# Kernel optimization log

Measured on AMD Instinct MI355X. Metric: run time of the kernel, lower is better.

The kernel has to match this reference:

```python
import jax, jax.numpy as jnp
import numpy as np
import math

S, B, D = 2048, 8, 256
HEADS = 8
DPROJ = 128
DFF = 1024
DH = DPROJ // HEADS  # 16


def _layernorm(x, g, b, eps=1e-5):
    mu = jnp.mean(x, axis=-1, keepdims=True)
    var = jnp.mean((x - mu) ** 2, axis=-1, keepdims=True)
    return (x - mu) * jax.lax.rsqrt(var + eps) * g + b


def setup_inputs() -> dict:
    key = jax.random.key(0)
    ks = jax.random.split(key, 16)
    s = 0.02
    return {
        "src": jax.random.normal(ks[0], (S, B, D), dtype=jnp.float32),
        "Wq": jax.random.normal(ks[1], (D, DPROJ), dtype=jnp.float32) * s,
        "bq": jnp.zeros((DPROJ,), dtype=jnp.float32),
        "Wk": jax.random.normal(ks[2], (D, DPROJ), dtype=jnp.float32) * s,
        "bk": jnp.zeros((DPROJ,), dtype=jnp.float32),
        "Wv": jax.random.normal(ks[3], (D, DPROJ), dtype=jnp.float32) * s,
        "bv": jnp.zeros((DPROJ,), dtype=jnp.float32),
        "Wo": jax.random.normal(ks[4], (DPROJ, D), dtype=jnp.float32) * s,
        "ln1_g": jnp.ones((D,), dtype=jnp.float32),
        "ln1_b": jnp.zeros((D,), dtype=jnp.float32),
        "W1": jax.random.normal(ks[5], (D, DFF), dtype=jnp.float32) * s,
        "b1": jnp.zeros((DFF,), dtype=jnp.float32),
        "W2": jax.random.normal(ks[6], (DFF, D), dtype=jnp.float32) * s,
        "b2": jnp.zeros((D,), dtype=jnp.float32),
        "ln2_g": jnp.ones((D,), dtype=jnp.float32),
        "ln2_b": jnp.zeros((D,), dtype=jnp.float32),
    }


def reference(src, Wq, bq, Wk, bk, Wv, bv, Wo, ln1_g, ln1_b, W1, b1, W2, b2, ln2_g, ln2_b):
    # src: (S, B, D)
    q = src @ Wq + bq  # (S, B, DPROJ)
    k = src @ Wk + bk
    v = src @ Wv + bv

    # _reshape_to_batches: (S, B, h*dh) -> (S, B*h, dh), then sdpa moves batch first
    def split_heads(x):
        return jnp.transpose(x.reshape(S, B * HEADS, DH), (1, 0, 2))  # (B*h, S, dh)

    qh, kh, vh = split_heads(q), split_heads(k), split_heads(v)
    scores = jnp.einsum('bid,bjd->bij', qh, kh) / math.sqrt(DH)  # (B*h, S, S)
    attn = jax.nn.softmax(scores, axis=-1)
    ctx = jnp.einsum('bij,bjd->bid', attn, vh)  # (B*h, S, dh)

    # _reshape_from_batches: (B*h, S, dh) -> (S, B, DPROJ)
    ctx = jnp.transpose(ctx, (1, 0, 2)).reshape(S, B, DPROJ)
    y = ctx @ Wo  # (S, B, D), no bias

    x = _layernorm(src + y, ln1_g, ln1_b)
    ffn = jax.nn.relu(x @ W1 + b1) @ W2 + b2
    return _layernorm(x + ffn, ln2_g, ln2_b)
```

## Files before the change

### kernel.cpp

```cpp
#include <hip/hip_runtime.h>
#include <math.h>

#define SLEN 2048
#define BATCH 8
#define DMODEL 256
#define HEADS 8
#define DPROJ 128
#define DFF 1024
#define DH 16
#define MROWS (SLEN*BATCH)

typedef unsigned short u16;
typedef unsigned int u32;
typedef __attribute__((ext_vector_type(8))) short short8;
typedef __attribute__((ext_vector_type(4))) float f32x4;
typedef __attribute__((ext_vector_type(16))) float f32x16;
typedef __attribute__((ext_vector_type(4))) unsigned short u16x4;

__device__ __forceinline__ u16 f2bf(float x) {
    union { float f; u32 u; } v; v.f = x;
    u32 r = v.u + 0x7FFFu + ((v.u >> 16) & 1u);
    return (u16)(r >> 16);
}
__device__ __forceinline__ float bf2f(u16 h) {
    union { u32 u; float f; } v; v.u = ((u32)h) << 16;
    return v.f;
}
__device__ __forceinline__ float fexp2(float x) { return __builtin_amdgcn_exp2f(x); }
__device__ __forceinline__ u32 pack_bf(float lo, float hi) {
    union { float f; u32 u; } a, b; a.f = lo; b.f = hi;
    return __builtin_amdgcn_perm(b.u, a.u, 0x07060302u);
}
__device__ __forceinline__ void gld16(const u16* g, u16* l) {
    __builtin_amdgcn_global_load_lds(
        (const __attribute__((address_space(1))) void*)g,
        (__attribute__((address_space(3))) void*)l, 16, 0, 0);
}

__global__ void prep_kernel(const float* __restrict__ src, u16* __restrict__ srcb,
                            const float* __restrict__ Wq, const float* __restrict__ Wk,
                            const float* __restrict__ Wv, const float* __restrict__ Wo,
                            const float* __restrict__ W1, const float* __restrict__ W2,
                            u16* __restrict__ WqT, u16* __restrict__ WkT,
                            u16* __restrict__ WvT, u16* __restrict__ WoT,
                            u16* __restrict__ W1T, u16* __restrict__ W2T,
                            u16* __restrict__ va) {
    if (blockIdx.x < 4096) {
        int idx = (blockIdx.x * 256 + threadIdx.x) * 4;
        float4 v = *(const float4*)(src + idx);
        u16x4 o;
        o.x = f2bf(v.x); o.y = f2bf(v.y); o.z = f2bf(v.z); o.w = f2bf(v.w);
        *(u16x4*)(srcb + idx) = o;
        return;
    }
    int i = (blockIdx.x - 4096) * 256 + threadIdx.x;
    if (i < 32768) {
        int n = i >> 8, k = i & 255;
        WqT[i] = f2bf(Wq[k * 128 + n]);
    } else if (i < 65536) {
        int j = i - 32768; int n = j >> 8, k = j & 255;
        WkT[j] = f2bf(Wk[k * 128 + n]);
    } else if (i < 98304) {
        int j = i - 65536; int n = j >> 8, k = j & 255;
        WvT[j] = f2bf(Wv[k * 128 + n]);
    } else if (i < 131072) {
        int j = i - 98304; int n = j >> 7, k = j & 127;
        WoT[j] = f2bf(Wo[k * 256 + n]);
    } else if (i < 393216) {
        int j = i - 131072; int n = j >> 8, k = j & 255;
        W1T[j] = f2bf(W1[k * 1024 + n]);
    } else if (i < 655360) {
        int j = i - 393216; int n = j >> 10, k = j & 1023;
        W2T[j] = f2bf(W2[k * 256 + n]);
    } else if (i < 786432) {
        int j = i - 655360; int bh = j >> 11, col = j & 2047;
        va[(size_t)bh * 65536 + 16 * 2048 + col] = (u16)0x3F80;
    }
}

template<int BN, bool RELU, bool HAS_BIAS, bool OUT_BF16>
__global__ void mfma_gemm(const u16* __restrict__ A, const u16* __restrict__ BT,
                          const float* __restrict__ bias, void* __restrict__ Cout,
                          int M, int N, int K) {
    constexpr int NJ = BN / 32;
    __shared__ __align__(16) u16 As[128 * 32];
    __shared__ __align__(16) u16 Bs[BN * 32];
    const int tid = threadIdx.x;
    const int row0 = blockIdx.x * 128;
    const int col0 = blockIdx.y * BN;
    const int w = tid >> 6, l = tid & 63;
    const int wr = (w & 1) * 64, wc = (w >> 1) * (BN / 2);
    const int lcol = l & 15, lrow = (l >> 4) * 4, g = l >> 4;
    const int sl = l >> 2;
    const int swc = ((l & 3) ^ (sl & 3)) * 8;
    const int fsw = (g ^ (lcol & 3)) * 8;

    const u16* Ag0 = A + (size_t)(row0 + 16 * w + sl) * K + swc;
    const u16* Ag1 = Ag0 + (size_t)64 * K;
    const u16* Bg0 = BT + (size_t)(col0 + 16 * w + sl) * K + swc;
    const u16* Bg1 = Bg0 + (size_t)64 * K;
    u16* lA0 = As + (16 * w) * 32;
    u16* lA1 = As + (16 * w + 64) * 32;
    u16* lB0 = Bs + (16 * w) * 32;
    u16* lB1 = Bs + (16 * w + 64) * 32;

    f32x4 acc[4][NJ] = {};
    for (int k0 = 0; k0 < K; k0 += 32) {
        gld16(Ag0 + k0, lA0);
        gld16(Ag1 + k0, lA1);
        gld16(Bg0 + k0, lB0);
        if (BN == 128) gld16(Bg1 + k0, lB1);
        __syncthreads();
        short8 af[4], bf[NJ];
        #pragma unroll
        for (int i = 0; i < 4; ++i)
            af[i] = *(const short8*)(As + (wr + i * 16 + lcol) * 32 + fsw);
        #pragma unroll
        for (int j = 0; j < NJ; ++j)
            bf[j] = *(const short8*)(Bs + (wc + j * 16 + lcol) * 32 + fsw);
        #pragma unroll
        for (int i = 0; i < 4; ++i)
            #pragma unroll
            for (int j = 0; j < NJ; ++j)
                acc[i][j] = __builtin_amdgcn_mfma_f32_16x16x32_bf16(
                    af[i], bf[j], acc[i][j], 0, 0, 0);
        __syncthreads();
    }
    float bv[NJ];
    #pragma unroll
    for (int j = 0; j < NJ; ++j)
        bv[j] = HAS_BIAS ? bias[col0 + wc + j * 16 + lcol] : 0.f;
    #pragma unroll
    for (int i = 0; i < 4; ++i) {
        #pragma unroll
        for (int r = 0; r < 4; ++r) {
            size_t grow = row0 + wr + i * 16 + lrow + r;
            #pragma unroll
            for (int j = 0; j < NJ; ++j) {
                int gcol = col0 + wc + j * 16 + lcol;
                float c = acc[i][j][r] + bv[j];
                if (RELU) c = fmaxf(c, 0.f);
                if (OUT_BF16) ((u16*)Cout)[grow * N + gcol] = f2bf(c);
                else          ((float*)Cout)[grow * N + gcol] = c;
            }
        }
    }
}

__global__ void qkv_mfma(const u16* __restrict__ A,
                         const u16* __restrict__ WqT, const u16* __restrict__ WkT,
                         const u16* __restrict__ WvT,
                         const float* __restrict__ bq, const float* __restrict__ bk,
                         const float* __restrict__ bv,
                         u16* __restrict__ qhp, u16* __restrict__ khp,
                         u16* __restrict__ va) {
    const int which = blockIdx.z;
    const u16* BT   = which == 0 ? WqT : (which == 1 ? WkT : WvT);
    const float* bs = which == 0 ? bq : (which == 1 ? bk : bv);
    const float scale = which == 0 ? 0.25f * 1.44269504f : 1.0f;
    __shared__ __align__(16) u16 As[128 * 32];
    __shared__ __align__(16) u16 Bs[128 * 32];
    const int tid = threadIdx.x;
    const int row0 = blockIdx.x * 128;
    const int w = tid >> 6, l = tid & 63;
    const int wr = (w & 1) * 64, wc = (w >> 1) * 64;
    const int lcol = l & 15, lrow = (l >> 4) * 4, g = l >> 4;
    const int sl = l >> 2;
    const int swc = ((l & 3) ^ (sl & 3)) * 8;
    const int fsw = (g ^ (lcol & 3)) * 8;

    const u16* Ag0 = A + (size_t)(row0 + 16 * w + sl) * DMODEL + swc;
    const u16* Ag1 = Ag0 + (size_t)64 * DMODEL;
    const u16* Bg0 = BT + (size_t)(16 * w + sl) * DMODEL + swc;
    const u16* Bg1 = Bg0 + (size_t)64 * DMODEL;
    u16* lA0 = As + (16 * w) * 32;
    u16* lA1 = As + (16 * w + 64) * 32;
    u16* lB0 = Bs + (16 * w) * 32;
    u16* lB1 = Bs + (16 * w + 64) * 32;

    f32x4 acc[4][4] = {};
    for (int k0 = 0; k0 < DMODEL; k0 += 32) {
        gld16(Ag0 + k0, lA0);
        gld16(Ag1 + k0, lA1);
        gld16(Bg0 + k0, lB0);
        gld16(Bg1 + k0, lB1);
        __syncthreads();
        short8 af[4], bf[4];
        #pragma unroll
        for (int i = 0; i < 4; ++i)
            af[i] = *(const short8*)(As + (wr + i * 16 + lcol) * 32 + fsw);
        #pragma unroll
        for (int j = 0; j < 4; ++j)
            bf[j] = *(const short8*)(Bs + (wc + j * 16 + lcol) * 32 + fsw);
        #pragma unroll
        for (int i = 0; i < 4; ++i)
            #pragma unroll
            for (int j = 0; j < 4; ++j)
                acc[i][j] = __builtin_amdgcn_mfma_f32_16x16x32_bf16(
                    af[i], bf[j], acc[i][j], 0, 0, 0);
        __syncthreads();
    }
    #pragma unroll
    for (int i = 0; i < 4; ++i) {
        #pragma unroll
        for (int r = 0; r < 4; ++r) {
            int grow = row0 + wr + i * 16 + lrow + r;
            int b = grow & 7, s = grow >> 3;
            #pragma unroll
            for (int j = 0; j < 4; ++j) {
                int gcol = wc + j * 16 + lcol;
                int h = gcol >> 4, d = gcol & 15;
                float c = acc[i][j][r] + bs[gcol];
                if (which == 2) {
                    va[((size_t)(b * 8 + h) * 32 + d) * SLEN + s] = f2bf(c);
                } else {
                    u16* outp = which == 0 ? qhp : khp;
                    outp[((size_t)(b * 8 + h) * SLEN + s) * 16 + d] = f2bf(c * scale);
                }
            }
        }
    }
}

__global__ __launch_bounds__(128, 4)
void attn_mfma(const u16* __restrict__ qg, const u16* __restrict__ kg,
               const u16* __restrict__ va, u16* __restrict__ ctx) {
    __shared__ __align__(16) u16 Ps[2 * 32 * 68];
    const int bh = blockIdx.y;
    const int tid = threadIdx.x;
    const int w = tid >> 6, l = tid & 63;
    const int n = l & 31, h5 = l >> 5;
    u16* Pw = Ps + w * (32 * 68);

    const int qbase = blockIdx.x * 64 + w * 32;
    const short8 qf = *(const short8*)(
        qg + ((size_t)bh * SLEN + qbase + n) * 16 + h5 * 8);
    const u16* kb = kg + (size_t)bh * SLEN * 16;
    const u16* vb = va + ((size_t)bh * 32 + n) * SLEN + h5 * 8;

    f32x16 oacc = {};
    short8 kf0 = *(const short8*)(kb + (size_t)n * 16 + h5 * 8);
    short8 kf1 = *(const short8*)(kb + (size_t)(32 + n) * 16 + h5 * 8);
    short8 vf[4];
    #pragma unroll
    for (int st = 0; st < 4; ++st)
        vf[st] = *(const short8*)(vb + st * 16);

    for (int kt = 0; kt < 32; ++kt) {
        const int k0 = kt * 64;
        f32x16 z = {};
        f32x16 s0 = __builtin_amdgcn_mfma_f32_32x32x16_bf16(kf0, qf, z, 0, 0, 0);
        f32x16 s1 = __builtin_amdgcn_mfma_f32_32x32x16_bf16(kf1, qf, z, 0, 0, 0);
        const int kn = (k0 + 64) & (SLEN - 1);
        short8 kf0n = *(const short8*)(kb + (size_t)(kn + n) * 16 + h5 * 8);
        short8 kf1n = *(const short8*)(kb + (size_t)(kn + 32 + n) * 16 + h5 * 8);
        short8 vfn[4];
        #pragma unroll
        for (int st = 0; st < 4; ++st)
            vfn[st] = *(const short8*)(vb + kn + st * 16);
        #pragma unroll
        for (int r4 = 0; r4 < 4; ++r4) {
            uint2 d;
            d.x = pack_bf(fexp2(s0[r4 * 4 + 0]), fexp2(s0[r4 * 4 + 1]));
            d.y = pack_bf(fexp2(s0[r4 * 4 + 2]), fexp2(s0[r4 * 4 + 3]));
            *(uint2*)(Pw + n * 68 + 8 * r4 + 4 * h5) = d;
        }
        #pragma unroll
        for (int r4 = 0; r4 < 4; ++r4) {
            uint2 d;
            d.x = pack_bf(fexp2(s1[r4 * 4 + 0]), fexp2(s1[r4 * 4 + 1]));
            d.y = pack_bf(fexp2(s1[r4 * 4 + 2]), fexp2(s1[r4 * 4 + 3]));
            *(uint2*)(Pw + n * 68 + 32 + 8 * r4 + 4 * h5) = d;
        }
        #pragma unroll
        for (int st = 0; st < 4; ++st) {
            const u16* rp = Pw + n * 68 + st * 16 + h5 * 8;
            union { uint2 q2[2]; short8 v; } ap;
            ap.q2[0] = *(const uint2*)rp;
            ap.q2[1] = *(const uint2*)(rp + 4);
            oacc = __builtin_amdgcn_mfma_f32_32x32x16_bf16(ap.v, vf[st], oacc, 0, 0, 0);
        }
        kf0 = kf0n; kf1 = kf1n;
        #pragma unroll
        for (int st = 0; st < 4; ++st) vf[st] = vfn[st];
    }
    float* Ob = (float*)Pw;
    if (n <= 16) {
        #pragma unroll
        for (int r = 0; r < 16; ++r) {
            int qq = (r & 3) + 8 * (r >> 2) + 4 * h5;
            Ob[qq * 20 + n] = oacc[r];
        }
    }
    __syncthreads();
    const int q = l >> 1, half = l & 1;
    f32x4 o0 = *(const f32x4*)(Ob + q * 20 + half * 8);
    f32x4 o1 = *(const f32x4*)(Ob + q * 20 + half * 8 + 4);
    float rcp = 1.0f / Ob[q * 20 + 16];
    u16x4 p0, p1;
    p0.x = f2bf(o0[0] * rcp); p0.y = f2bf(o0[1] * rcp);
    p0.z = f2bf(o0[2] * rcp); p0.w = f2bf(o0[3] * rcp);
    p1.x = f2bf(o1[0] * rcp); p1.y = f2bf(o1[1] * rcp);
    p1.z = f2bf(o1[2] * rcp); p1.w = f2bf(o1[3] * rcp);
    const int b = bh >> 3, h = bh & 7;
    const int qrow = qbase + q;
    u16* dst = ctx + ((size_t)qrow * BATCH + b) * DPROJ + h * DH + half * 8;
    *(u16x4*)dst = p0;
    *(u16x4*)(dst + 4) = p1;
}

__global__ void ln1_kernel(const u16* __restrict__ srcb, const u16* __restrict__ y,
                           const float* __restrict__ g, const float* __restrict__ bb,
                           u16* __restrict__ xb) {
    const int w = threadIdx.x >> 6, l = threadIdx.x & 63;
    const int row = blockIdx.x * 4 + w;
    const int c = l * 4;
    size_t base = (size_t)row * DMODEL;
    u16x4 s4 = *(const u16x4*)(srcb + base + c);
    u16x4 y4 = *(const u16x4*)(y + base + c);
    float v[4] = { bf2f(s4.x) + bf2f(y4.x), bf2f(s4.y) + bf2f(y4.y),
                   bf2f(s4.z) + bf2f(y4.z), bf2f(s4.w) + bf2f(y4.w) };
    float sum = v[0] + v[1] + v[2] + v[3];
    float ss  = v[0]*v[0] + v[1]*v[1] + v[2]*v[2] + v[3]*v[3];
    #pragma unroll
    for (int off = 1; off < 64; off <<= 1) {
        sum += __shfl_xor(sum, off);
        ss  += __shfl_xor(ss, off);
    }
    float mu = sum * (1.0f / 256.0f);
    float var = ss * (1.0f / 256.0f) - mu * mu;
    float rs = rsqrtf(var + 1e-5f);
    float4 g4 = *(const float4*)(g + c);
    float4 b4 = *(const float4*)(bb + c);
    u16x4 o;
    o.x = f2bf((v[0] - mu) * rs * g4.x + b4.x);
    o.y = f2bf((v[1] - mu) * rs * g4.y + b4.y);
    o.z = f2bf((v[2] - mu) * rs * g4.z + b4.z);
    o.w = f2bf((v[3] - mu) * rs * g4.w + b4.w);
    *(u16x4*)(xb + base + c) = o;
}

__global__ void ln2_kernel(const u16* __restrict__ x, const u16* __restrict__ f,
                           const float* __restrict__ g, const float* __restrict__ bb,
                           float* __restrict__ out) {
    const int w = threadIdx.x >> 6, l = threadIdx.x & 63;
    const int row = blockIdx.x * 4 + w;
    const int c = l * 4;
    size_t base = (size_t)row * DMODEL;
    u16x4 x4 = *(const u16x4*)(x + base + c);
    u16x4 f4 = *(const u16x4*)(f + base + c);
    float v[4] = { bf2f(x4.x) + bf2f(f4.x), bf2f(x4.y) + bf2f(f4.y),
                   bf2f(x4.z) + bf2f(f4.z), bf2f(x4.w) + bf2f(f4.w) };
    float sum = v[0] + v[1] + v[2] + v[3];
    float ss  = v[0]*v[0] + v[1]*v[1] + v[2]*v[2] + v[3]*v[3];
    #pragma unroll
    for (int off = 1; off < 64; off <<= 1) {
        sum += __shfl_xor(sum, off);
        ss  += __shfl_xor(ss, off);
    }
    float mu = sum * (1.0f / 256.0f);
    float var = ss * (1.0f / 256.0f) - mu * mu;
    float rs = rsqrtf(var + 1e-5f);
    float4 g4 = *(const float4*)(g + c);
    float4 b4 = *(const float4*)(bb + c);
    float4 o;
    o.x = (v[0] - mu) * rs * g4.x + b4.x;
    o.y = (v[1] - mu) * rs * g4.y + b4.y;
    o.z = (v[2] - mu) * rs * g4.z + b4.z;
    o.w = (v[3] - mu) * rs * g4.w + b4.w;
    *(float4*)(out + base + c) = o;
}

extern "C" void kernel_launch(void* const* d_in, const int* in_sizes, int n_in,
                              void* d_out, int out_size, void* d_ws, size_t ws_size,
                              hipStream_t stream) {
    const float* src = (const float*)d_in[0];
    const float* Wq  = (const float*)d_in[1];
    const float* bq  = (const float*)d_in[2];
    const float* Wk  = (const float*)d_in[3];
    const float* bk  = (const float*)d_in[4];
    const float* Wv  = (const float*)d_in[5];
    const float* bv  = (const float*)d_in[6];
    const float* Wo  = (const float*)d_in[7];
    const float* g1  = (const float*)d_in[8];
    const float* be1 = (const float*)d_in[9];
    const float* W1  = (const float*)d_in[10];
    const float* b1  = (const float*)d_in[11];
    const float* W2  = (const float*)d_in[12];
    const float* b2  = (const float*)d_in[13];
    const float* g2  = (const float*)d_in[14];
    const float* be2 = (const float*)d_in[15];
    char* ws = (char*)d_ws;
    float* out = (float*)d_out;

    u16* qhp  = (u16*)(ws + 0);
    u16* khp  = (u16*)(ws + 4194304);
    u16* vaug = (u16*)(ws + 8388608);
    u16* ctxb = (u16*)(ws + 16777216);
    u16* yb   = (u16*)(ws + 20971520);
    u16* hb   = (u16*)(ws + 0);
    u16* xb   = (u16*)(ws + 33554432);
    u16* fb   = (u16*)(ws + 41943040);
    u16* srcb = (u16*)(ws + 50331648);
    u16* WqT  = (u16*)(ws + 58720256);
    u16* WkT  = (u16*)(ws + 58785792);
    u16* WvT  = (u16*)(ws + 58851328);
    u16* WoT  = (u16*)(ws + 58916864);
    u16* W1T  = (u16*)(ws + 58982400);
    u16* W2T  = (u16*)(ws + 59506688);

    prep_kernel<<<7168, 256, 0, stream>>>(src, srcb, Wq, Wk, Wv, Wo, W1, W2,
                                          WqT, WkT, WvT, WoT, W1T, W2T, vaug);
    qkv_mfma<<<dim3(128, 1, 3), 256, 0, stream>>>(srcb, WqT, WkT, WvT,
                                                  bq, bk, bv, qhp, khp, vaug);
    attn_mfma<<<dim3(32, 64), 128, 0, stream>>>(qhp, khp, vaug, ctxb);
    mfma_gemm<64, false, false, true><<<dim3(128, 4), 256, 0, stream>>>(
        ctxb, WoT, nullptr, yb, MROWS, DMODEL, DPROJ);
    ln1_kernel<<<MROWS / 4, 256, 0, stream>>>(srcb, yb, g1, be1, xb);
    mfma_gemm<128, true, true, true><<<dim3(128, 8), 256, 0, stream>>>(
        xb, W1T, b1, hb, MROWS, DFF, DMODEL);
    mfma_gemm<64, false, true, true><<<dim3(128, 4), 256, 0, stream>>>(
        hb, W2T, b2, fb, MROWS, DMODEL, DFF);
    ln2_kernel<<<MROWS / 4, 256, 0, stream>>>(xb, fb, g2, be2, out);
}
```

Before: 240.6 us.

## Split attention key range across two waves per query tile and reduce partials in LDS

The attention kernel now launches 256 threads per block. Each pair of waves shares a 32-query tile, and each wave of the pair processes half of the key sequence. This doubles the number of waves working in parallel on the same grid, aiming to raise occupancy and latency hiding in the exp/MFMA loop. The partial unnormalized outputs and row sums are combined through shared memory before normalization. In exchange the kernel gains an extra barrier, a shared-memory reduction and double the LDS footprint per block. This works without max-subtraction because the softmax uses plain exp2.

```diff
diff --git a/kernel.cpp b/kernel.cpp
--- a/kernel.cpp
+++ b/kernel.cpp
@@ -222,36 +222,38 @@
     }
 }
 
-__global__ __launch_bounds__(128, 4)
+__global__ __launch_bounds__(256, 4)
 void attn_mfma(const u16* __restrict__ qg, const u16* __restrict__ kg,
                const u16* __restrict__ va, u16* __restrict__ ctx) {
-    __shared__ __align__(16) u16 Ps[2 * 32 * 68];
+    __shared__ __align__(16) u16 Ps[4 * 32 * 68];
     const int bh = blockIdx.y;
     const int tid = threadIdx.x;
     const int w = tid >> 6, l = tid & 63;
+    const int qw = w & 1, kw = w >> 1;
     const int n = l & 31, h5 = l >> 5;
     u16* Pw = Ps + w * (32 * 68);
 
-    const int qbase = blockIdx.x * 64 + w * 32;
+    const int qbase = blockIdx.x * 64 + qw * 32;
     const short8 qf = *(const short8*)(
         qg + ((size_t)bh * SLEN + qbase + n) * 16 + h5 * 8);
     const u16* kb = kg + (size_t)bh * SLEN * 16;
     const u16* vb = va + ((size_t)bh * 32 + n) * SLEN + h5 * 8;
+    const int k00 = kw * (SLEN / 2);
 
     f32x16 oacc = {};
-    short8 kf0 = *(const short8*)(kb + (size_t)n * 16 + h5 * 8);
-    short8 kf1 = *(const short8*)(kb + (size_t)(32 + n) * 16 + h5 * 8);
+    short8 kf0 = *(const short8*)(kb + (size_t)(k00 + n) * 16 + h5 * 8);
+    short8 kf1 = *(const short8*)(kb + (size_t)(k00 + 32 + n) * 16 + h5 * 8);
     short8 vf[4];
     #pragma unroll
     for (int st = 0; st < 4; ++st)
-        vf[st] = *(const short8*)(vb + st * 16);
-
-    for (int kt = 0; kt < 32; ++kt) {
-        const int k0 = kt * 64;
+        vf[st] = *(const short8*)(vb + k00 + st * 16);
+
+    for (int kt = 0; kt < 16; ++kt) {
+        const int k0 = k00 + kt * 64;
         f32x16 z = {};
         f32x16 s0 = __builtin_amdgcn_mfma_f32_32x32x16_bf16(kf0, qf, z, 0, 0, 0);
         f32x16 s1 = __builtin_amdgcn_mfma_f32_32x32x16_bf16(kf1, qf, z, 0, 0, 0);
-        const int kn = (k0 + 64) & (SLEN - 1);
+        const int kn = k00 + ((kt + 1) & 15) * 64;
         short8 kf0n = *(const short8*)(kb + (size_t)(kn + n) * 16 + h5 * 8);
         short8 kf1n = *(const short8*)(kb + (size_t)(kn + 32 + n) * 16 + h5 * 8);
         short8 vfn[4];
@@ -284,29 +286,45 @@
         #pragma unroll
         for (int st = 0; st < 4; ++st) vf[st] = vfn[st];
     }
-    float* Ob = (float*)Pw;
-    if (n <= 16) {
-        #pragma unroll
-        for (int r = 0; r < 16; ++r) {
-            int qq = (r & 3) + 8 * (r >> 2) + 4 * h5;
-            Ob[qq * 20 + n] = oacc[r];
-        }
-    }
+
+    float* Pf = (float*)Ps;
     __syncthreads();
-    const int q = l >> 1, half = l & 1;
-    f32x4 o0 = *(const f32x4*)(Ob + q * 20 + half * 8);
-    f32x4 o1 = *(const f32x4*)(Ob + q * 20 + half * 8 + 4);
-    float rcp = 1.0f / Ob[q * 20 + 16];
-    u16x4 p0, p1;
-    p0.x = f2bf(o0[0] * rcp); p0.y = f2bf(o0[1] * rcp);
-    p0.z = f2bf(o0[2] * rcp); p0.w = f2bf(o0[3] * rcp);
-    p1.x = f2bf(o1[0] * rcp); p1.y = f2bf(o1[1] * rcp);
-    p1.z = f2bf(o1[2] * rcp); p1.w = f2bf(o1[3] * rcp);
-    const int b = bh >> 3, h = bh & 7;
-    const int qrow = qbase + q;
-    u16* dst = ctx + ((size_t)qrow * BATCH + b) * DPROJ + h * DH + half * 8;
-    *(u16x4*)dst = p0;
-    *(u16x4*)(dst + 4) = p1;
+    if (kw == 1) {
+        float* part = Pf + qw * (32 * 20);
+        if (n <= 16) {
+            #pragma unroll
+            for (int r = 0; r < 16; ++r) {
+                int qq = (r & 3) + 8 * (r >> 2) + 4 * h5;
+                part[qq * 20 + n] = oacc[r];
+            }
+        }
+    }
+    __syncthreads();
+    if (kw == 0) {
+        const float* part = Pf + qw * (32 * 20);
+        float* Ob = Pf + 2560 + qw * (32 * 20);
+        if (n <= 16) {
+            #pragma unroll
+            for (int r = 0; r < 16; ++r) {
+                int qq = (r & 3) + 8 * (r >> 2) + 4 * h5;
+                Ob[qq * 20 + n] = oacc[r] + part[qq * 20 + n];
+            }
+        }
+        const int q = l >> 1, half = l & 1;
+        f32x4 o0 = *(const f32x4*)(Ob + q * 20 + half * 8);
+        f32x4 o1 = *(const f32x4*)(Ob + q * 20 + half * 8 + 4);
+        float rcp = 1.0f / Ob[q * 20 + 16];
+        u16x4 p0, p1;
+        p0.x = f2bf(o0[0] * rcp); p0.y = f2bf(o0[1] * rcp);
+        p0.z = f2bf(o0[2] * rcp); p0.w = f2bf(o0[3] * rcp);
+        p1.x = f2bf(o1[0] * rcp); p1.y = f2bf(o1[1] * rcp);
+        p1.z = f2bf(o1[2] * rcp); p1.w = f2bf(o1[3] * rcp);
+        const int b = bh >> 3, h = bh & 7;
+        const int qrow = qbase + q;
+        u16* dst = ctx + ((size_t)qrow * BATCH + b) * DPROJ + h * DH + half * 8;
+        *(u16x4*)dst = p0;
+        *(u16x4*)(dst + 4) = p1;
+    }
 }
 
 __global__ void ln1_kernel(const u16* __restrict__ srcb, const u16* __restrict__ y,
@@ -413,7 +431,7 @@
                                           WqT, WkT, WvT, WoT, W1T, W2T, vaug);
     qkv_mfma<<<dim3(128, 1, 3), 256, 0, stream>>>(srcb, WqT, WkT, WvT,
                                                   bq, bk, bv, qhp, khp, vaug);
-    attn_mfma<<<dim3(32, 64), 128, 0, stream>>>(qhp, khp, vaug, ctxb);
+    attn_mfma<<<dim3(32, 64), 256, 0, stream>>>(qhp, khp, vaug, ctxb);
     mfma_gemm<64, false, false, true><<<dim3(128, 4), 256, 0, stream>>>(
         ctxb, WoT, nullptr, yb, MROWS, DMODEL, DPROJ);
     ln1_kernel<<<MROWS / 4, 256, 0, stream>>>(srcb, yb, g1, be1, xb);
```

Result: no change. 245.2 us (+1.9%).
